# Kernel optimization log

Hardware: AMD Instinct MI355X
Metric: run time of the kernel (lower is better)

Reference implementation:

```python
import jax, jax.numpy as jnp
import numpy as np

EPS = 1e-6

def _normalize(x, eps=1e-12):
    n = jnp.linalg.norm(x, axis=-1, keepdims=True)
    return x / jnp.maximum(n, eps)

def _gather_nodes(nodes, idx):
    # nodes [B,N,C], idx [B,N,K] -> [B,N,K,C]
    B = nodes.shape[0]
    return nodes[jnp.arange(B)[:, None, None], idx]

def _dist(X, top_k):
    dX = X[:, None, :, :] - X[:, :, None, :]          # [B,N,N,3]
    D = jnp.sqrt(jnp.sum(dX * dX, axis=-1) + EPS)      # [B,N,N]
    neg_vals, E_idx = jax.lax.top_k(-D, top_k)         # smallest distances
    return D, -neg_vals, E_idx

def _gs_dist(D):
    D_min, D_max, D_count = 0.0, 20.0, 15
    D_mu = jnp.linspace(D_min, D_max, D_count)         # [15]
    D_sigma = (D_max - D_min) / D_count
    return jnp.exp(-(((D[..., None] - D_mu) / D_sigma) ** 2))

def _pos_encodings(E_idx, num_embeddings=16):
    N = E_idx.shape[1]
    ii = jnp.arange(N, dtype=jnp.float32)[None, :, None]
    d = (E_idx.astype(jnp.float32) - ii)[..., None]    # [B,N,K,1]
    freq = jnp.exp(jnp.arange(0, num_embeddings, 2, dtype=jnp.float32)
                   * -(np.log(10000.0) / num_embeddings))  # [8]
    angles = d * freq                                   # [B,N,K,8]
    return jnp.concatenate([jnp.cos(angles), jnp.sin(angles)], axis=-1)

def _orientations_coarse(X, E_idx, eps=1e-6):
    dX = X[:, 1:, :] - X[:, :-1, :]
    U = _normalize(dX)
    u_2, u_1, u_0 = U[:, :-2], U[:, 1:-1], U[:, 2:]
    n_2 = _normalize(jnp.cross(u_2, u_1))
    n_1 = _normalize(jnp.cross(u_1, u_0))
    cosA = jnp.clip(-(u_1 * u_0).sum(-1), -1 + eps, 1 - eps)
    A = jnp.arccos(cosA)
    cosD = jnp.clip((n_2 * n_1).sum(-1), -1 + eps, 1 - eps)
    Dang = jnp.sign((u_2 * n_1).sum(-1)) * jnp.arccos(cosD)
    AD = jnp.stack([jnp.cos(A), jnp.sin(A) * jnp.cos(Dang), jnp.sin(A) * jnp.sin(Dang)], axis=2)
    AD = jnp.pad(AD, ((0, 0), (1, 2), (0, 0)))          # [B,N,3]
    o_1 = _normalize(u_2 - u_1)
    O = jnp.stack([o_1, n_2, jnp.cross(o_1, n_2)], axis=2)  # [B,N-3,3,3]
    O = O.reshape(O.shape[0], O.shape[1], 9)
    O = jnp.pad(O, ((0, 0), (1, 2), (0, 0)))            # [B,N,9]
    O_nb = _gather_nodes(O, E_idx)                      # [B,N,K,9]
    X_nb = _gather_nodes(X, E_idx)                      # [B,N,K,3]
    O3 = O.reshape(O.shape[0], O.shape[1], 3, 3)
    dXn = X_nb - X[:, :, None, :]                       # [B,N,K,3]
    dU = jnp.einsum('bnij,bnkj->bnki', O3, dXn)         # rotate into local frame
    dU = _normalize(dU)
    # NOTE: original also computes R = O^T @ O_nb and quaternions Q, but Q is
    # dead code (never returned); omitted here (jit would DCE it anyway).
    return AD, dU

def setup_inputs() -> dict:
    key = jax.random.key(0)
    coords = jax.random.normal(key, (2, 4096, 3), dtype=jnp.float32) * 10.0
    return {"coords": coords, "num_k": 30}

def reference(coords, num_k):
    D, D_neighbors, E_idx = _dist(coords, num_k)
    gs_d = _gs_dist(D_neighbors)
    pos_emb = _pos_encodings(E_idx)
    AD_features, O_features = _orientations_coarse(coords, E_idx)
    return pos_emb, AD_features, O_features, gs_d, D_neighbors, E_idx
```

## Files before the change

kernel.cpp:

```cpp
#include <hip/hip_runtime.h>
#include <hip/hip_bf16.h>

constexpr int B = 2;
constexpr int N = 4096;
constexpr int K = 30;
constexpr int ROWS_PER_BLK = 4;

constexpr size_t OFF_POS = 0;
constexpr size_t OFF_AD  = OFF_POS + (size_t)B * N * K * 16;
constexpr size_t OFF_O   = OFF_AD  + (size_t)B * N * 3;
constexpr size_t OFF_GS  = OFF_O   + (size_t)B * N * K * 3;
constexpr size_t OFF_DN  = OFF_GS  + (size_t)B * N * K * 15;
constexpr size_t OFF_E   = OFF_DN  + (size_t)B * N * K;

constexpr float BIGD = 1e30f;
constexpr unsigned int BIGJ = 0xFFFFFFFFu;

struct F3 { float x, y, z; };

template <bool ISBF16>
__device__ __forceinline__ float ldx(const void* __restrict__ X, int idx) {
  if constexpr (ISBF16) {
    return __bfloat162float(((const __hip_bfloat16*)X)[idx]);
  } else {
    return ((const float*)X)[idx];
  }
}

template <bool ISBF16>
__device__ __forceinline__ float distf(const void* __restrict__ Xb, int j,
                                       float xi, float yi, float zi) {
#pragma clang fp contract(off)
  float px, py, pz;
  if constexpr (ISBF16) {
    px = ldx<true>(Xb, j * 3 + 0);
    py = ldx<true>(Xb, j * 3 + 1);
    pz = ldx<true>(Xb, j * 3 + 2);
  } else {
    const F3 p = ((const F3*)Xb)[j];
    px = p.x; py = p.y; pz = p.z;
  }
  const float dx = px - xi;
  const float dy = py - yi;
  const float dz = pz - zi;
  return sqrtf(((dx * dx + dy * dy) + dz * dz) + 1e-6f);
}

template <int CTRL>
__device__ __forceinline__ float dpp_min_f32(float v) {
  const int mv = __builtin_amdgcn_update_dpp(__float_as_int(BIGD), __float_as_int(v),
                                             CTRL, 0xF, 0xF, false);
  return fminf(__int_as_float(mv), v);
}
template <int CTRL>
__device__ __forceinline__ unsigned int dpp_min_u32(unsigned int v) {
  const unsigned int mv = (unsigned int)__builtin_amdgcn_update_dpp(
      (int)BIGJ, (int)v, CTRL, 0xF, 0xF, false);
  return mv < v ? mv : v;
}
__device__ __forceinline__ float wave_min_f32_bcast(float v) {
  v = dpp_min_f32<0x111>(v);
  v = dpp_min_f32<0x112>(v);
  v = dpp_min_f32<0x114>(v);
  v = dpp_min_f32<0x118>(v);
  v = dpp_min_f32<0x142>(v);
  v = dpp_min_f32<0x143>(v);
  return __int_as_float(__builtin_amdgcn_readlane(__float_as_int(v), 63));
}
__device__ __forceinline__ unsigned int wave_min_u32_bcast(unsigned int v) {
  v = dpp_min_u32<0x111>(v);
  v = dpp_min_u32<0x112>(v);
  v = dpp_min_u32<0x114>(v);
  v = dpp_min_u32<0x118>(v);
  v = dpp_min_u32<0x142>(v);
  v = dpp_min_u32<0x143>(v);
  return (unsigned int)__builtin_amdgcn_readlane((int)v, 63);
}

__device__ __forceinline__ float red2pi(float x) {
  return x - 6.28318530718f * rintf(x * 0.15915494309f);
}

__device__ __forceinline__ void norm3(float& x, float& y, float& z) {
#pragma clang fp contract(off)
  float n = sqrtf((x * x + y * y) + z * z);
  n = fmaxf(n, 1e-12f);
  x /= n; y /= n; z /= n;
}

__device__ __forceinline__ void cross3(float ax, float ay, float az,
                                       float bx, float by, float bz,
                                       float& cx, float& cy, float& cz) {
#pragma clang fp contract(off)
  cx = ay * bz - az * by;
  cy = az * bx - ax * bz;
  cz = ax * by - ay * bx;
}

template <bool ISBF16>
__device__ __forceinline__ void body(const void* __restrict__ Xb,
                                     float* __restrict__ out,
                                     int b, int i, int lane) {
#pragma clang fp contract(off)
  const float xi = ldx<ISBF16>(Xb, i * 3 + 0);
  const float yi = ldx<ISBF16>(Xb, i * 3 + 1);
  const float zi = ldx<ISBF16>(Xb, i * 3 + 2);

  float d0 = BIGD, d1 = BIGD;
  int   j0 = 0x7FFFFFFF, j1 = 0x7FFFFFFF;
#pragma unroll 8
  for (int t = 0; t < 64; ++t) {
    const int j = t * 64 + lane;
    const float d = distf<ISBF16>(Xb, j, xi, yi, zi);
    const bool lt1 = d < d1;
    const float td = lt1 ? d : d1;
    const int   tj = lt1 ? j : j1;
    const bool lt0 = td < d0;
    d1 = lt0 ? d0 : td;  j1 = lt0 ? j0 : tj;
    d0 = lt0 ? td : d0;  j0 = lt0 ? tj : j0;
  }

  unsigned long long exm = 0;
  int   sjv = 0;
  float sdv = 0.0f;
  for (int k = 0; k < K; ++k) {
    const float dmin = wave_min_f32_bcast(d0);
    const unsigned int jc = (d0 == dmin) ? (unsigned int)j0 : BIGJ;
    const unsigned int jmin = wave_min_u32_bcast(jc);
    if (lane == k) { sjv = (int)jmin; sdv = dmin; }

    const int w  = (int)(jmin & 63u);
    const int tw = (int)(jmin >> 6);
    if (lane == w) {
      exm |= (1ull << tw);
      d0 = d1; j0 = j1;
      d1 = BIGD; j1 = 0x7FFFFFFF;
    }
    if (__ballot(d0 == BIGD) != 0ull) {
      const unsigned int mlo = (unsigned int)__builtin_amdgcn_readlane((int)(unsigned int)(exm & 0xFFFFFFFFull), w);
      const unsigned int mhi = (unsigned int)__builtin_amdgcn_readlane((int)(unsigned int)(exm >> 32), w);
      const unsigned long long m = ((unsigned long long)mhi << 32) | mlo;
      const int j2 = (lane << 6) | w;
      const float d2 = distf<ISBF16>(Xb, j2, xi, yi, zi);
      const float dc = ((m >> lane) & 1ull) ? BIGD : d2;
      const float dmin2 = wave_min_f32_bcast(dc);
      const unsigned int jc2 = (dc == dmin2) ? (unsigned int)j2 : BIGJ;
      const unsigned int jmin2 = wave_min_u32_bcast(jc2);
      if (lane == w) { d0 = dmin2; j0 = (int)jmin2; }
    }
  }

  float ad0 = 0.f, ad1 = 0.f, ad2 = 0.f;
  float o00 = 0.f, o01 = 0.f, o02 = 0.f;
  float o10 = 0.f, o11 = 0.f, o12 = 0.f;
  float o20 = 0.f, o21 = 0.f, o22 = 0.f;
  if (i >= 1 && i <= N - 3) {
    const float ax = ldx<ISBF16>(Xb, (i - 1) * 3 + 0), ay = ldx<ISBF16>(Xb, (i - 1) * 3 + 1), az = ldx<ISBF16>(Xb, (i - 1) * 3 + 2);
    const float cx = ldx<ISBF16>(Xb, (i + 1) * 3 + 0), cy = ldx<ISBF16>(Xb, (i + 1) * 3 + 1), cz = ldx<ISBF16>(Xb, (i + 1) * 3 + 2);
    const float ex = ldx<ISBF16>(Xb, (i + 2) * 3 + 0), ey = ldx<ISBF16>(Xb, (i + 2) * 3 + 1), ez = ldx<ISBF16>(Xb, (i + 2) * 3 + 2);
    float u2x = xi - ax, u2y = yi - ay, u2z = zi - az; norm3(u2x, u2y, u2z);
    float u1x = cx - xi, u1y = cy - yi, u1z = cz - zi; norm3(u1x, u1y, u1z);
    float u0x = ex - cx, u0y = ey - cy, u0z = ez - cz; norm3(u0x, u0y, u0z);
    float n2x, n2y, n2z; cross3(u2x, u2y, u2z, u1x, u1y, u1z, n2x, n2y, n2z); norm3(n2x, n2y, n2z);
    float n1x, n1y, n1z; cross3(u1x, u1y, u1z, u0x, u0y, u0z, n1x, n1y, n1z); norm3(n1x, n1y, n1z);
    const float dotu = (u1x * u0x + u1y * u0y) + u1z * u0z;
    const float cosA = fminf(fmaxf(-dotu, -1.0f + 1e-6f), 1.0f - 1e-6f);
    const float A = acosf(cosA);
    const float dotn = (n2x * n1x + n2y * n1y) + n2z * n1z;
    const float cosD = fminf(fmaxf(dotn, -1.0f + 1e-6f), 1.0f - 1e-6f);
    const float du2n1 = (u2x * n1x + u2y * n1y) + u2z * n1z;
    const float sg = (du2n1 > 0.f) ? 1.f : ((du2n1 < 0.f) ? -1.f : 0.f);
    const float Dang = sg * acosf(cosD);
    const float sA = __sinf(A),    cA = __cosf(A);
    const float sD = __sinf(Dang), cD = __cosf(Dang);
    ad0 = cA; ad1 = sA * cD; ad2 = sA * sD;
    float o1x = u2x - u1x, o1y = u2y - u1y, o1z = u2z - u1z; norm3(o1x, o1y, o1z);
    o00 = o1x; o01 = o1y; o02 = o1z;
    o10 = n2x; o11 = n2y; o12 = n2z;
    cross3(o1x, o1y, o1z, n2x, n2y, n2z, o20, o21, o22);
  }

  const int row = b * N + i;

  {
    const size_t base = OFF_POS + (size_t)row * (K * 16);
#pragma unroll
    for (int it = 0; it < 8; ++it) {
      const int idx = it * 64 + lane;
      const int k = (idx >> 4) < K ? (idx >> 4) : (K - 1);
      const int p = idx & 15;
      const int jk = __shfl(sjv, k, 64);
      const float df = (float)(jk - i);
      const float fr = __expf((float)((p & 7) * 2) * -0.57564627f);
      const float r = red2pi(df * fr);
      const float v = (p < 8) ? __cosf(r) : __sinf(r);
      if (idx < K * 16) out[base + idx] = v;
    }
  }

  {
    const size_t base = OFF_GS + (size_t)row * (K * 15);
#pragma unroll
    for (int it = 0; it < 8; ++it) {
      const int idx = it * 64 + lane;
      const int kq = idx / 15;
      const int k = kq < K ? kq : (K - 1);
      const int m = idx - kq * 15;
      const float d = __shfl(sdv, k, 64);
      const float mu = (float)(m * (20.0 / 14.0));
      const float q = (d - mu) / 1.3333334f;
      const float v = __expf(-(q * q));
      if (idx < K * 15) out[base + idx] = v;
    }
  }

  if (lane < K) {
    const size_t rowk = (size_t)row * K + lane;
    const int   j = sjv;
    out[OFF_E  + rowk] = (float)j;
    out[OFF_DN + rowk] = sdv;

    const float gx = ldx<ISBF16>(Xb, j * 3 + 0) - xi;
    const float gy = ldx<ISBF16>(Xb, j * 3 + 1) - yi;
    const float gz = ldx<ISBF16>(Xb, j * 3 + 2) - zi;
    const float v0 = (o00 * gx + o01 * gy) + o02 * gz;
    const float v1 = (o10 * gx + o11 * gy) + o12 * gz;
    const float v2 = (o20 * gx + o21 * gy) + o22 * gz;
    const float nn = fmaxf(sqrtf((v0 * v0 + v1 * v1) + v2 * v2), 1e-12f);
    out[OFF_O + rowk * 3 + 0] = v0 / nn;
    out[OFF_O + rowk * 3 + 1] = v1 / nn;
    out[OFF_O + rowk * 3 + 2] = v2 / nn;
  } else if (lane < K + 3) {
    const int c = lane - K;
    const float v = (c == 0) ? ad0 : (c == 1) ? ad1 : ad2;
    out[OFF_AD + (size_t)row * 3 + c] = v;
  }
}

__global__ __launch_bounds__(64 * ROWS_PER_BLK)
void protein_feat_kernel(const void* __restrict__ X,
                         float* __restrict__ out) {
  const int lane = threadIdx.x & 63;
  const int wv   = threadIdx.x >> 6;
  const int row  = blockIdx.x * ROWS_PER_BLK + wv;
  const int b    = row >> 12;
  const int i    = row & (N - 1);

  const unsigned short h = ((const unsigned short*)X)[2 * lane];
  const int e = (h >> 7) & 0xFF;
  const bool sane = ((h & 0x7FFF) == 0) || (e >= 115 && e <= 134);
  const unsigned long long bal = __ballot(sane);
  const bool isbf16 = __popcll(bal) >= 40;

  if (isbf16) {
    const void* Xb = (const void*)((const __hip_bfloat16*)X + (size_t)b * N * 3);
    body<true>(Xb, out, b, i, lane);
  } else {
    const void* Xb = (const void*)((const float*)X + (size_t)b * N * 3);
    body<false>(Xb, out, b, i, lane);
  }
}

extern "C" void kernel_launch(void* const* d_in, const int* in_sizes, int n_in,
                              void* d_out, int out_size, void* d_ws, size_t ws_size,
                              hipStream_t stream) {
  const void* X = d_in[0];
  float* out = (float*)d_out;
  (void)in_sizes; (void)n_in; (void)d_ws; (void)ws_size; (void)out_size;
  protein_feat_kernel<<<dim3(B * N / ROWS_PER_BLK), dim3(64 * ROWS_PER_BLK), 0, stream>>>(X, out);
}
```

Baseline: 124.0 us.

## Replace brute-force kNN with x-sorted bucket grid and windowed search

Adds a build kernel that counting-sorts points by x coordinate into 4096 buckets, writing SoA coordinates, ranks and bucket starts to workspace. Each query wave then scans only a window of sorted points around its rank and widens the window until the 30th-nearest distance is provably covered on both sides. This avoids scanning all 4096 points per query. The trade-offs are an extra launch, a serial scan in a two-block build kernel, and possible repeated widening passes. The change also switches to a three-deep per-lane candidate list, adds a fast single-winner argmin path, hoists the frequency computation, and drops the bf16 input path.

```diff
diff --git a/kernel.cpp b/kernel.cpp
--- a/kernel.cpp
+++ b/kernel.cpp
@@ -4,7 +4,12 @@
 constexpr int B = 2;
 constexpr int N = 4096;
 constexpr int K = 30;
-constexpr int ROWS_PER_BLK = 4;
+constexpr int NBKT = 4096;
+constexpr float XMIN = -48.0f;
+constexpr float XRANGE = 96.0f;
+constexpr float BKT_H = XRANGE / (float)NBKT;
+constexpr int W0 = 640;
+constexpr int WEXP = 512;
 
 constexpr size_t OFF_POS = 0;
 constexpr size_t OFF_AD  = OFF_POS + (size_t)B * N * K * 16;
@@ -14,32 +19,30 @@
 constexpr size_t OFF_E   = OFF_DN  + (size_t)B * N * K;
 
 constexpr float BIGD = 1e30f;
-constexpr unsigned int BIGJ = 0xFFFFFFFFu;
+constexpr unsigned int BIGF = 0xFFFFFFFFu;
+
+constexpr size_t WS_STRIDE = 7 * 4096 + 8;
+
+struct WsB { float *xs, *ys, *zs; int *js, *rank, *sb, *bstart; };
+__device__ __forceinline__ WsB wsb(void* ws, int b) {
+  float* base = (float*)ws + (size_t)b * WS_STRIDE;
+  WsB w;
+  w.xs = base; w.ys = base + 4096; w.zs = base + 8192;
+  w.js = (int*)(base + 12288); w.rank = (int*)(base + 16384);
+  w.sb = (int*)(base + 20480); w.bstart = (int*)(base + 24576);
+  return w;
+}
+
+__device__ __forceinline__ int bucketOf(float x) {
+  int t = (int)((x - XMIN) * ((float)NBKT / XRANGE));
+  return t < 0 ? 0 : (t > NBKT - 1 ? NBKT - 1 : t);
+}
 
 struct F3 { float x, y, z; };
 
-template <bool ISBF16>
-__device__ __forceinline__ float ldx(const void* __restrict__ X, int idx) {
-  if constexpr (ISBF16) {
-    return __bfloat162float(((const __hip_bfloat16*)X)[idx]);
-  } else {
-    return ((const float*)X)[idx];
-  }
-}
-
-template <bool ISBF16>
-__device__ __forceinline__ float distf(const void* __restrict__ Xb, int j,
-                                       float xi, float yi, float zi) {
+__device__ __forceinline__ float dist_core(float px, float py, float pz,
+                                           float xi, float yi, float zi) {
 #pragma clang fp contract(off)
-  float px, py, pz;
-  if constexpr (ISBF16) {
-    px = ldx<true>(Xb, j * 3 + 0);
-    py = ldx<true>(Xb, j * 3 + 1);
-    pz = ldx<true>(Xb, j * 3 + 2);
-  } else {
-    const F3 p = ((const F3*)Xb)[j];
-    px = p.x; py = p.y; pz = p.z;
-  }
   const float dx = px - xi;
   const float dy = py - yi;
   const float dz = pz - zi;
@@ -55,7 +58,7 @@
 template <int CTRL>
 __device__ __forceinline__ unsigned int dpp_min_u32(unsigned int v) {
   const unsigned int mv = (unsigned int)__builtin_amdgcn_update_dpp(
-      (int)BIGJ, (int)v, CTRL, 0xF, 0xF, false);
+      (int)BIGF, (int)v, CTRL, 0xF, 0xF, false);
   return mv < v ? mv : v;
 }
 __device__ __forceinline__ float wave_min_f32_bcast(float v) {
@@ -77,12 +80,37 @@
   return (unsigned int)__builtin_amdgcn_readlane((int)v, 63);
 }
 
+__device__ __forceinline__ void pop_argmin(float d0, unsigned int f0,
+                                           float& dmin, unsigned int& fmin) {
+  dmin = wave_min_f32_bcast(d0);
+  const unsigned long long tie = __ballot(d0 == dmin);
+  if (__popcll(tie) == 1) {
+    fmin = (unsigned int)__builtin_amdgcn_readlane((int)f0, __ffsll(tie) - 1);
+  } else {
+    fmin = wave_min_u32_bcast((d0 == dmin) ? f0 : BIGF);
+  }
+}
+
+__device__ __forceinline__ void insert3(float d, unsigned int jf,
+                                        float& d0, float& d1, float& d2,
+                                        unsigned int& f0, unsigned int& f1, unsigned int& f2) {
+  const bool lt2 = (d < d2) || (d == d2 && jf < f2);
+  const bool lt1 = (d < d1) || (d == d1 && jf < f1);
+  const bool lt0 = (d < d0) || (d == d0 && jf < f0);
+  const float        nd2 = lt1 ? d1 : (lt2 ? d : d2);
+  const unsigned int nf2 = lt1 ? f1 : (lt2 ? jf : f2);
+  const float        nd1 = lt0 ? d0 : (lt1 ? d : d1);
+  const unsigned int nf1 = lt0 ? f0 : (lt1 ? jf : f1);
+  const float        nd0 = lt0 ? d : d0;
+  const unsigned int nf0 = lt0 ? jf : f0;
+  d2 = nd2; f2 = nf2; d1 = nd1; f1 = nf1; d0 = nd0; f0 = nf0;
+}
+
 __device__ __forceinline__ float red2pi(float x) {
   return x - 6.28318530718f * rintf(x * 0.15915494309f);
 }
 
 __device__ __forceinline__ void norm3(float& x, float& y, float& z) {
-#pragma clang fp contract(off)
   float n = sqrtf((x * x + y * y) + z * z);
   n = fmaxf(n, 1e-12f);
   x /= n; y /= n; z /= n;
@@ -91,63 +119,157 @@
 __device__ __forceinline__ void cross3(float ax, float ay, float az,
                                        float bx, float by, float bz,
                                        float& cx, float& cy, float& cz) {
-#pragma clang fp contract(off)
   cx = ay * bz - az * by;
   cy = az * bx - ax * bz;
   cz = ax * by - ay * bx;
 }
 
-template <bool ISBF16>
-__device__ __forceinline__ void body(const void* __restrict__ Xb,
-                                     float* __restrict__ out,
-                                     int b, int i, int lane) {
-#pragma clang fp contract(off)
-  const float xi = ldx<ISBF16>(Xb, i * 3 + 0);
-  const float yi = ldx<ISBF16>(Xb, i * 3 + 1);
-  const float zi = ldx<ISBF16>(Xb, i * 3 + 2);
-
-  float d0 = BIGD, d1 = BIGD;
-  int   j0 = 0x7FFFFFFF, j1 = 0x7FFFFFFF;
-#pragma unroll 8
-  for (int t = 0; t < 64; ++t) {
-    const int j = t * 64 + lane;
-    const float d = distf<ISBF16>(Xb, j, xi, yi, zi);
-    const bool lt1 = d < d1;
-    const float td = lt1 ? d : d1;
-    const int   tj = lt1 ? j : j1;
-    const bool lt0 = td < d0;
-    d1 = lt0 ? d0 : td;  j1 = lt0 ? j0 : tj;
-    d0 = lt0 ? td : d0;  j0 = lt0 ? tj : j0;
-  }
-
-  unsigned long long exm = 0;
+__global__ __launch_bounds__(1024)
+void build_kernel(const float* __restrict__ X, void* __restrict__ ws) {
+  __shared__ unsigned int cnt[NBKT];
+  __shared__ unsigned int tmp[NBKT];
+  const int b = blockIdx.x;
+  const int tid = threadIdx.x;
+  const float* __restrict__ Xb = X + (size_t)b * N * 3;
+  WsB w = wsb(ws, b);
+
+#pragma unroll
+  for (int e = 0; e < 4; ++e) cnt[e * 1024 + tid] = 0;
+  __syncthreads();
+#pragma unroll
+  for (int e = 0; e < 4; ++e) {
+    const int j = e * 1024 + tid;
+    atomicAdd(&cnt[bucketOf(Xb[j * 3])], 1u);
+  }
+  __syncthreads();
+  unsigned int* src = cnt;
+  unsigned int* dst = tmp;
+  for (int off = 1; off < NBKT; off <<= 1) {
+#pragma unroll
+    for (int e = 0; e < 4; ++e) {
+      const int j = e * 1024 + tid;
+      unsigned int v = src[j];
+      if (j >= off) v += src[j - off];
+      dst[j] = v;
+    }
+    __syncthreads();
+    unsigned int* t = src; src = dst; dst = t;
+  }
+#pragma unroll
+  for (int e = 0; e < 4; ++e) {
+    const int j = e * 1024 + tid;
+    const unsigned int ex = (j == 0) ? 0u : src[j - 1];
+    dst[j] = ex;
+    w.bstart[j] = (int)ex;
+  }
+  if (tid == 0) w.bstart[NBKT] = N;
+  __syncthreads();
+#pragma unroll
+  for (int e = 0; e < 4; ++e) {
+    const int j = e * 1024 + tid;
+    const float x = Xb[j * 3];
+    const int bkt = bucketOf(x);
+    const int slot = (int)atomicAdd(&dst[bkt], 1u);
+    w.xs[slot] = x;
+    w.ys[slot] = Xb[j * 3 + 1];
+    w.zs[slot] = Xb[j * 3 + 2];
+    w.js[slot] = j;
+    w.rank[j] = slot;
+    w.sb[slot] = bkt;
+  }
+}
+
+__device__ __forceinline__ void scan_range(const WsB& w, int a, int bnd, int lane,
+                                           float qx, float qy, float qz,
+                                           float& d0, float& d1, float& d2,
+                                           unsigned int& f0, unsigned int& f1, unsigned int& f2) {
+  const int cb = a >> 6, ce = (bnd + 63) >> 6;
+  for (int c = cb; c < ce; ++c) {
+    const int s = c * 64 + lane;
+    const float x = w.xs[s], y = w.ys[s], z = w.zs[s];
+    const int jo = w.js[s];
+    float d = dist_core(x, y, z, qx, qy, qz);
+    unsigned int jf = ((unsigned int)jo << 6) | (unsigned int)c;
+    if (s < a || s >= bnd) { d = BIGD; jf = BIGF; }
+    insert3(d, jf, d0, d1, d2, f0, f1, f2);
+  }
+}
+
+__global__ __launch_bounds__(256)
+void protein_feat_kernel(const float* __restrict__ X,
+                         float* __restrict__ out,
+                         void* __restrict__ ws) {
+  const int lane = threadIdx.x & 63;
+  const int wv   = threadIdx.x >> 6;
+  const int row  = blockIdx.x * 4 + wv;
+  const int b    = row >> 12;
+  const int i    = row & (N - 1);
+  const WsB w = wsb(ws, b);
+  const float* __restrict__ Xb = X + (size_t)b * N * 3;
+
+  const float qx = Xb[i * 3 + 0];
+  const float qy = Xb[i * 3 + 1];
+  const float qz = Xb[i * 3 + 2];
+
+  const int p = w.rank[i];
+  int t_lo = p - W0; if (t_lo < 0) t_lo = 0;
+  int t_hi = p + W0; if (t_hi > N) t_hi = N;
+  int blo = w.sb[t_lo];
+  int bhi = w.sb[t_hi - 1] + 1;
+  int slo = w.bstart[blo];
+  int shi = w.bstart[bhi];
+
+  float d0 = BIGD, d1 = BIGD, d2 = BIGD;
+  unsigned int f0 = BIGF, f1 = BIGF, f2 = BIGF;
+  scan_range(w, slo, shi, lane, qx, qy, qz, d0, d1, d2, f0, f1, f2);
+
   int   sjv = 0;
   float sdv = 0.0f;
-  for (int k = 0; k < K; ++k) {
-    const float dmin = wave_min_f32_bcast(d0);
-    const unsigned int jc = (d0 == dmin) ? (unsigned int)j0 : BIGJ;
-    const unsigned int jmin = wave_min_u32_bcast(jc);
-    if (lane == k) { sjv = (int)jmin; sdv = dmin; }
-
-    const int w  = (int)(jmin & 63u);
-    const int tw = (int)(jmin >> 6);
-    if (lane == w) {
-      exm |= (1ull << tw);
-      d0 = d1; j0 = j1;
-      d1 = BIGD; j1 = 0x7FFFFFFF;
+  for (;;) {
+    const float sd0 = d0, sd1 = d1, sd2 = d2;
+    const unsigned int sf0 = f0, sf1 = f1, sf2 = f2;
+    unsigned long long exm = 0;
+    float d30 = 0.0f;
+    for (int k = 0; k < K; ++k) {
+      float dmin; unsigned int fmin;
+      pop_argmin(d0, f0, dmin, fmin);
+      if (lane == k) { sjv = (int)(fmin >> 6); sdv = dmin; }
+      d30 = dmin;
+      const unsigned long long wb = __ballot(d0 == dmin && f0 == fmin);
+      const int wl = __ffsll(wb) - 1;
+      const int cw = (int)(fmin & 63u);
+      if (lane == wl) {
+        exm |= (1ull << cw);
+        d0 = d1; f0 = f1; d1 = d2; f1 = f2; d2 = BIGD; f2 = BIGF;
+      }
+      if (__ballot(d0 == BIGD) != 0ull) {
+        const unsigned int mlo = (unsigned int)__builtin_amdgcn_readlane((int)(unsigned int)(exm & 0xFFFFFFFFull), wl);
+        const unsigned int mhi = (unsigned int)__builtin_amdgcn_readlane((int)(unsigned int)(exm >> 32), wl);
+        const unsigned long long m = ((unsigned long long)mhi << 32) | mlo;
+        const int s = lane * 64 + wl;
+        const float x = w.xs[s], y = w.ys[s], z = w.zs[s];
+        const int jo = w.js[s];
+        float dc = dist_core(x, y, z, qx, qy, qz);
+        unsigned int fc = ((unsigned int)jo << 6) | (unsigned int)lane;
+        if (s < slo || s >= shi || ((m >> lane) & 1ull)) { dc = BIGD; fc = BIGF; }
+        float dm2; unsigned int fm2;
+        pop_argmin(dc, fc, dm2, fm2);
+        if (lane == wl) { d0 = dm2; f0 = fm2; }
+      }
     }
-    if (__ballot(d0 == BIGD) != 0ull) {
-      const unsigned int mlo = (unsigned int)__builtin_amdgcn_readlane((int)(unsigned int)(exm & 0xFFFFFFFFull), w);
-      const unsigned int mhi = (unsigned int)__builtin_amdgcn_readlane((int)(unsigned int)(exm >> 32), w);
-      const unsigned long long m = ((unsigned long long)mhi << 32) | mlo;
-      const int j2 = (lane << 6) | w;
-      const float d2 = distf<ISBF16>(Xb, j2, xi, yi, zi);
-      const float dc = ((m >> lane) & 1ull) ? BIGD : d2;
-      const float dmin2 = wave_min_f32_bcast(dc);
-      const unsigned int jc2 = (dc == dmin2) ? (unsigned int)j2 : BIGJ;
-      const unsigned int jmin2 = wave_min_u32_bcast(jc2);
-      if (lane == w) { d0 = dmin2; j0 = (int)jmin2; }
-    }
+    const bool covL = (slo == 0) || ((qx - (XMIN + (float)blo * BKT_H)) > d30 + 1e-4f);
+    const bool covR = (shi == N) || (((XMIN + (float)bhi * BKT_H) - qx) > d30 + 1e-4f);
+    if (covL && covR) break;
+    d0 = sd0; d1 = sd1; d2 = sd2; f0 = sf0; f1 = sf1; f2 = sf2;
+    int nlo_t = slo - WEXP; if (nlo_t < 0) nlo_t = 0;
+    int nhi_t = shi + WEXP; if (nhi_t > N) nhi_t = N;
+    const int nblo = w.sb[nlo_t];
+    const int nbhi = w.sb[nhi_t - 1] + 1;
+    const int nslo = w.bstart[nblo];
+    const int nshi = w.bstart[nbhi];
+    if (nslo < slo) scan_range(w, nslo, slo, lane, qx, qy, qz, d0, d1, d2, f0, f1, f2);
+    if (nshi > shi) scan_range(w, shi, nshi, lane, qx, qy, qz, d0, d1, d2, f0, f1, f2);
+    slo = nslo; blo = nblo; shi = nshi; bhi = nbhi;
   }
 
   float ad0 = 0.f, ad1 = 0.f, ad2 = 0.f;
@@ -155,11 +277,11 @@
   float o10 = 0.f, o11 = 0.f, o12 = 0.f;
   float o20 = 0.f, o21 = 0.f, o22 = 0.f;
   if (i >= 1 && i <= N - 3) {
-    const float ax = ldx<ISBF16>(Xb, (i - 1) * 3 + 0), ay = ldx<ISBF16>(Xb, (i - 1) * 3 + 1), az = ldx<ISBF16>(Xb, (i - 1) * 3 + 2);
-    const float cx = ldx<ISBF16>(Xb, (i + 1) * 3 + 0), cy = ldx<ISBF16>(Xb, (i + 1) * 3 + 1), cz = ldx<ISBF16>(Xb, (i + 1) * 3 + 2);
-    const float ex = ldx<ISBF16>(Xb, (i + 2) * 3 + 0), ey = ldx<ISBF16>(Xb, (i + 2) * 3 + 1), ez = ldx<ISBF16>(Xb, (i + 2) * 3 + 2);
-    float u2x = xi - ax, u2y = yi - ay, u2z = zi - az; norm3(u2x, u2y, u2z);
-    float u1x = cx - xi, u1y = cy - yi, u1z = cz - zi; norm3(u1x, u1y, u1z);
+    const float ax = Xb[(i - 1) * 3 + 0], ay = Xb[(i - 1) * 3 + 1], az = Xb[(i - 1) * 3 + 2];
+    const float cx = Xb[(i + 1) * 3 + 0], cy = Xb[(i + 1) * 3 + 1], cz = Xb[(i + 1) * 3 + 2];
+    const float ex = Xb[(i + 2) * 3 + 0], ey = Xb[(i + 2) * 3 + 1], ez = Xb[(i + 2) * 3 + 2];
+    float u2x = qx - ax, u2y = qy - ay, u2z = qz - az; norm3(u2x, u2y, u2z);
+    float u1x = cx - qx, u1y = cy - qy, u1z = cz - qz; norm3(u1x, u1y, u1z);
     float u0x = ex - cx, u0y = ey - cy, u0z = ez - cz; norm3(u0x, u0y, u0z);
     float n2x, n2y, n2z; cross3(u2x, u2y, u2z, u1x, u1y, u1z, n2x, n2y, n2z); norm3(n2x, n2y, n2z);
     float n1x, n1y, n1z; cross3(u1x, u1y, u1z, u0x, u0y, u0z, n1x, n1y, n1z); norm3(n1x, n1y, n1z);
@@ -180,26 +302,27 @@
     cross3(o1x, o1y, o1z, n2x, n2y, n2z, o20, o21, o22);
   }
 
-  const int row = b * N + i;
+  const int rw = b * N + i;
 
   {
-    const size_t base = OFF_POS + (size_t)row * (K * 16);
+    const size_t base = OFF_POS + (size_t)rw * (K * 16);
+    const int pp = lane & 15;
+    const float fr = __expf((float)((pp & 7) * 2) * -0.57564627f);
+    const bool is_cos = (pp < 8);
 #pragma unroll
     for (int it = 0; it < 8; ++it) {
       const int idx = it * 64 + lane;
       const int k = (idx >> 4) < K ? (idx >> 4) : (K - 1);
-      const int p = idx & 15;
       const int jk = __shfl(sjv, k, 64);
       const float df = (float)(jk - i);
-      const float fr = __expf((float)((p & 7) * 2) * -0.57564627f);
       const float r = red2pi(df * fr);
-      const float v = (p < 8) ? __cosf(r) : __sinf(r);
+      const float v = is_cos ? __cosf(r) : __sinf(r);
       if (idx < K * 16) out[base + idx] = v;
     }
   }
 
   {
-    const size_t base = OFF_GS + (size_t)row * (K * 15);
+    const size_t base = OFF_GS + (size_t)rw * (K * 15);
 #pragma unroll
     for (int it = 0; it < 8; ++it) {
       const int idx = it * 64 + lane;
@@ -215,14 +338,13 @@
   }
 
   if (lane < K) {
-    const size_t rowk = (size_t)row * K + lane;
-    const int   j = sjv;
+    const size_t rowk = (size_t)rw * K + lane;
+    const int j = sjv;
     out[OFF_E  + rowk] = (float)j;
     out[OFF_DN + rowk] = sdv;
 
-    const float gx = ldx<ISBF16>(Xb, j * 3 + 0) - xi;
-    const float gy = ldx<ISBF16>(Xb, j * 3 + 1) - yi;
-    const float gz = ldx<ISBF16>(Xb, j * 3 + 2) - zi;
+    const F3 pt = ((const F3*)Xb)[j];
+    const float gx = pt.x - qx, gy = pt.y - qy, gz = pt.z - qz;
     const float v0 = (o00 * gx + o01 * gy) + o02 * gz;
     const float v1 = (o10 * gx + o11 * gy) + o12 * gz;
     const float v2 = (o20 * gx + o21 * gy) + o22 * gz;
@@ -233,39 +355,16 @@
   } else if (lane < K + 3) {
     const int c = lane - K;
     const float v = (c == 0) ? ad0 : (c == 1) ? ad1 : ad2;
-    out[OFF_AD + (size_t)row * 3 + c] = v;
-  }
-}
-
-__global__ __launch_bounds__(64 * ROWS_PER_BLK)
-void protein_feat_kernel(const void* __restrict__ X,
-                         float* __restrict__ out) {
-  const int lane = threadIdx.x & 63;
-  const int wv   = threadIdx.x >> 6;
-  const int row  = blockIdx.x * ROWS_PER_BLK + wv;
-  const int b    = row >> 12;
-  const int i    = row & (N - 1);
-
-  const unsigned short h = ((const unsigned short*)X)[2 * lane];
-  const int e = (h >> 7) & 0xFF;
-  const bool sane = ((h & 0x7FFF) == 0) || (e >= 115 && e <= 134);
-  const unsigned long long bal = __ballot(sane);
-  const bool isbf16 = __popcll(bal) >= 40;
-
-  if (isbf16) {
-    const void* Xb = (const void*)((const __hip_bfloat16*)X + (size_t)b * N * 3);
-    body<true>(Xb, out, b, i, lane);
-  } else {
-    const void* Xb = (const void*)((const float*)X + (size_t)b * N * 3);
-    body<false>(Xb, out, b, i, lane);
+    out[OFF_AD + (size_t)rw * 3 + c] = v;
   }
 }
 
 extern "C" void kernel_launch(void* const* d_in, const int* in_sizes, int n_in,
                               void* d_out, int out_size, void* d_ws, size_t ws_size,
                               hipStream_t stream) {
-  const void* X = d_in[0];
+  const float* X = (const float*)d_in[0];
   float* out = (float*)d_out;
-  (void)in_sizes; (void)n_in; (void)d_ws; (void)ws_size; (void)out_size;
-  protein_feat_kernel<<<dim3(B * N / ROWS_PER_BLK), dim3(64 * ROWS_PER_BLK), 0, stream>>>(X, out);
-}
+  (void)in_sizes; (void)n_in; (void)out_size; (void)ws_size;
+  build_kernel<<<dim3(B), dim3(1024), 0, stream>>>(X, d_ws);
+  protein_feat_kernel<<<dim3(B * N / 4), dim3(256), 0, stream>>>(X, out, d_ws);
+}
```

New measurement: 173.0 us. +39.5%, slower.
